# Performance work log

Hardware: AMD Instinct MI355X
Metric: run time of the kernel (lower is better)

## Reference

```python
import jax, jax.numpy as jnp
import numpy as np

EPS_BIAS = 1e-6  # bias_epsilon

def _l2n(x, axis):
    # F.normalize: x / clamp_min(||x||, 1e-12)
    return x / jnp.maximum(jnp.linalg.norm(x, axis=axis, keepdims=True), 1e-12)

def _se3_W(w):
    # convex completion: rows sum to 1
    return jnp.concatenate([w, 1.0 - w.sum(-1, keepdims=True)], axis=-1)

def _vlin(v, W):
    # channel-mixing linear over dim 1 of [B, C, 3, N]
    return jnp.einsum('oc,bcdn->bodn', W, v)

def _vec_sub(v, w, b, se3):
    # sub VecLinear with s_in=s_out=0: linear + tiny normalized bias
    W = _se3_W(w) if se3 else w
    out = _vlin(v, W)
    bias = (_l2n(b, -1) * EPS_BIAS).reshape(1, -1, 1, 1)
    return out + bias

def _cev_norm(x):
    # channel_equi_vec_normalize
    d = _l2n(x, 2)
    n = jnp.linalg.norm(x, axis=2, keepdims=True)
    return d * _l2n(n, 1)

def setup_inputs() -> dict:
    key = jax.random.key(0)
    B, v_in, v_out, s_in, s_out, N = 8, 128, 128, 64, 64, 4096
    ks = jax.random.split(key, 16)
    def w(k, shape, fan):
        return jax.random.normal(k, shape, jnp.float32) / np.float32(np.sqrt(fan))
    return {
        'v_input': jax.random.normal(ks[0], (B, v_in, 3, N), jnp.float32),
        's_input': jax.random.normal(ks[1], (B, s_in, N), jnp.float32),
        'weight':   w(ks[2], (v_out, v_in - 1), v_in) + 1.0 / v_in,
        'sv_w':     w(ks[3], (v_out, s_in), s_in),
        'sv_b':     w(ks[4], (v_out,), s_in),
        'cross_w':  w(ks[5], (v_out, v_in - 1), v_in) + 1.0 / v_in,
        'cross_b':  jax.random.normal(ks[6], (v_out,), jnp.float32),
        'crossfc_w': w(ks[7], (v_out, 2 * v_out - 1), 2 * v_out) + 1.0 / (2 * v_out),
        'crossfc_b': jax.random.normal(ks[8], (v_out,), jnp.float32),
        'vsdir_w':  w(ks[9], (v_in, v_in), v_in),
        'vsdir_b':  jax.random.normal(ks[10], (v_in,), jnp.float32),
        'vs_w':     w(ks[11], (s_out, v_in), v_in),
        'vs_b':     w(ks[12], (s_out,), v_in),
        'ss_w':     w(ks[13], (s_out, s_in), s_in),
        'ss_b':     w(ks[14], (s_out,), s_in),
    }

def reference(v_input, s_input, weight, sv_w, sv_b, cross_w, cross_b,
              crossfc_w, crossfc_b, vsdir_w, vsdir_b, vs_w, vs_b, ss_w, ss_b):
    # --- vector linear (sim3/se3: convex weights) ---
    v_o = _vlin(v_input, _se3_W(weight))                      # [B, v_out, 3, N]
    # --- scalar -> vector invariant scale (normalized over channels) ---
    scale = jnp.einsum('os,bsn->bon', sv_w, s_input) + sv_b[None, :, None]
    scale = _l2n(scale, 1)                                    # [B, v_out, N]
    m = v_o.mean(axis=1, keepdims=True)
    v_o = (v_o - m) * scale[:, :, None, :] + m
    # --- cross-product branch ---
    v_dual = _vec_sub(v_input, cross_w, cross_b, True)
    dual_o = v_dual.mean(axis=1, keepdims=True)
    out_o = v_o.mean(axis=1, keepdims=True)
    v_cross = jnp.cross(_cev_norm(v_dual - dual_o), v_o - out_o, axis=2) + v_o
    v_o = _vec_sub(jnp.concatenate([v_cross, v_o], axis=1), crossfc_w, crossfc_b, True)
    # --- vector -> scalar (invariant) ---
    v_sR = v_input - v_input.mean(axis=1, keepdims=True)
    dual_dir = _l2n(_vec_sub(v_sR, vsdir_w, vsdir_b, False), 2)  # so3 sub-module
    s_from_v = _l2n((v_sR * dual_dir).sum(axis=2), 1)         # [B, v_in, N]
    s_from_v = jnp.einsum('oc,bcn->bon', vs_w, s_from_v) + vs_b[None, :, None]
    s_from_s = jnp.einsum('os,bsn->bon', ss_w, s_input) + ss_b[None, :, None]
    return v_o, s_from_s + s_from_v
```

## Files before the change

### kernel.cpp

```cpp
#include <hip/hip_runtime.h>

#define VOUT_ELEMS 12582912

typedef __attribute__((ext_vector_type(8))) short bf16x8;
typedef __attribute__((ext_vector_type(4))) float f32x4;

__device__ __forceinline__ unsigned short f2b(float f) {
  unsigned x = __float_as_uint(f);
  x = (x + 0x7FFFu + ((x >> 16) & 1u)) >> 16;
  return (unsigned short)x;
}
__device__ __forceinline__ float b2f(unsigned short u) {
  return __uint_as_float(((unsigned)u) << 16);
}
__device__ __forceinline__ unsigned pk2(float a, float b) {
  unsigned r;
  asm("v_cvt_pk_bf16_f32 %0, %1, %2" : "=v"(r) : "v"(a), "v"(b));
  return r;
}


__global__ void kprep0(const float* __restrict__ weight, const float* __restrict__ cross_w,
                       const float* __restrict__ crossfc_w, const float* __restrict__ vsdir_w,
                       const float* __restrict__ cross_b, const float* __restrict__ crossfc_b,
                       const float* __restrict__ vsdir_b, float* __restrict__ wsf)
{
  const int tid = threadIdx.x;
  const int l = tid & 63;
  const int wg = blockIdx.x*4 + (tid>>6);
#pragma unroll
  for (int k = 0; k < 2; ++k) {
    int o = wg*2 + k;
    float a = weight[o*127+l]  + ((l<63) ? weight[o*127+64+l]  : 0.f);
    float b = cross_w[o*127+l] + ((l<63) ? cross_w[o*127+64+l] : 0.f);
    float f = crossfc_w[o*255+l] + crossfc_w[o*255+64+l] + crossfc_w[o*255+128+l]
            + ((l<63) ? crossfc_w[o*255+192+l] : 0.f);
    float v = vsdir_w[o*128+l] + vsdir_w[o*128+64+l];
#pragma unroll
    for (int m = 1; m < 64; m <<= 1) {
      a += __shfl_xor(a,m,64); b += __shfl_xor(b,m,64);
      f += __shfl_xor(f,m,64); v += __shfl_xor(v,m,64);
    }
    if (l == 0) {
      wsf[384+o] = a; wsf[512+o] = b; wsf[640+o] = f; wsf[768+o] = v*(1.f/128.f);
    }
  }
  if (blockIdx.x == 0 && tid < 192) {
    const float* bsrc = (tid < 64) ? cross_b : (tid < 128 ? crossfc_b : vsdir_b);
    float a = 0.f;
    for (int i = l; i < 128; i += 64) { float t = bsrc[i]; a += t*t; }
#pragma unroll
    for (int m = 1; m < 64; m <<= 1) a += __shfl_xor(a,m,64);
    float nb = fmaxf(sqrtf(a), 1e-12f);
    for (int i = l; i < 128; i += 64)
      wsf[(tid>>6)*128 + i] = bsrc[i] / nb * 1e-6f;
  }
}

__global__ void kprep1(const float* __restrict__ weight, const float* __restrict__ sv_w,
                       const float* __restrict__ cross_w, const float* __restrict__ crossfc_w,
                       const float* __restrict__ vsdir_w, const float* __restrict__ vs_w,
                       const float* __restrict__ ss_w,
                       unsigned short* __restrict__ wsb, const float* __restrict__ wsf)
{
  const int stride = 64*256;
  const int base = blockIdx.x*256 + threadIdx.x;
  const float* rs1 = wsf+384; const float* rs2 = wsf+512;
  const float* rsF = wsf+640; const float* vdm = wsf+768;
  for (int i = base; i < 16384; i += stride) {
    int j=i&7, lane=(i>>3)&63, ks=(i>>9)&3, mt=i>>11;
    int o=16*mt+(lane&15), cc=32*ks+8*(lane>>4)+j;
    wsb[i]       = f2b(cc<127 ? weight[o*127+cc]  : 1.f-rs1[o]);
    wsb[16384+i] = f2b(cc<127 ? cross_w[o*127+cc] : 1.f-rs2[o]);
    wsb[65536+i] = f2b(vsdir_w[o*128+cc] - vdm[o]);
  }
  for (int i = base; i < 32768; i += stride) {
    int j=i&7, lane=(i>>3)&63, ks=(i>>9)&7, mt=i>>12;
    int o=16*mt+(lane&15), cc=32*ks+8*(lane>>4)+j;
    wsb[32768+i] = f2b(cc<255 ? crossfc_w[o*255+cc] : 1.f-rsF[o]);
  }
  for (int i = base; i < 8192; i += stride) {
    int j=i&7, lane=(i>>3)&63, ks=(i>>9)&1, mt=i>>10;
    int o=16*mt+(lane&15), s=32*ks+8*(lane>>4)+j;
    wsb[81920+i] = f2b(sv_w[o*64+s]);
  }
  for (int i = base; i < 8192; i += stride) {
    int j=i&7, lane=(i>>3)&63, ks=(i>>9)&3, mt=i>>11;
    int o=16*mt+(lane&15), c=32*ks+8*(lane>>4)+j;
    wsb[90112+i] = f2b(vs_w[o*128+c]);
  }
  for (int i = base; i < 4096; i += stride) {
    int j=i&7, lane=(i>>3)&63, ks=(i>>9)&1, mt=i>>10;
    int o=16*mt+(lane&15), s=32*ks+8*(lane>>4)+j;
    wsb[98304+i] = f2b(ss_w[o*64+s]);
  }
}

__global__ __launch_bounds__(512) __attribute__((amdgpu_waves_per_eu(4)))
void kmain(
    const float* __restrict__ v_in, const float* __restrict__ s_in,
    const float* __restrict__ sv_b, const float* __restrict__ vs_b,
    const float* __restrict__ ss_b,
    const unsigned short* __restrict__ wsb, const float* __restrict__ wsf,
    float* __restrict__ out_v, float* __restrict__ out_s)
{
  __shared__ __align__(16) unsigned char smem[32768];
  unsigned short* bfr = (unsigned short*)smem;
  float* gmx          = (float*)(smem + 12288);
  float (*gred)[16][8]  = (float(*)[16][8])(smem + 12480);
  unsigned short* sfr = (unsigned short*)(smem + 24576);
  unsigned short* vfr = (unsigned short*)(smem + 26624);
  float (*gred2)[16][8] = (float(*)[16][8])(smem + 30720);

  const int tid = threadIdx.x;
  const int w = tid >> 6, l = tid & 63, h = l >> 4, c15 = l & 15;
  const int n0 = blockIdx.x * 16;
  const size_t bb = blockIdx.y;
  const size_t vbase = bb*384*4096 + n0;
  const size_t sbase = bb*64*4096 + n0;

  if (tid < 384) {
    int i = tid;
    int q = i & 3, d = (i >> 2) % 3, cq = i / 12;
    const float* src = &v_in[vbase + (size_t)(4*cq*3 + d)*4096 + 4*q];
    float4 x0 = *(const float4*)(src);
    float4 x1 = *(const float4*)(src + 3*4096);
    float4 x2 = *(const float4*)(src + 6*4096);
    float4 x3 = *(const float4*)(src + 9*4096);
    int slot = (cq >> 3)*3 + d;
    int hh = (cq >> 1) & 3;
    int jp = 2*(cq & 1);
    unsigned* bp = (unsigned*)bfr + (slot*64 + 16*hh + 4*q)*4 + jp;
    float a0[4]={x0.x,x0.y,x0.z,x0.w}, a1[4]={x1.x,x1.y,x1.z,x1.w};
    float a2[4]={x2.x,x2.y,x2.z,x2.w}, a3[4]={x3.x,x3.y,x3.z,x3.w};
#pragma unroll
    for (int e=0;e<4;++e)
      *(uint2*)(bp + e*4) = make_uint2(pk2(a0[e],a1[e]), pk2(a2[e],a3[e]));
  } else if (tid < 448) {
    int st = tid - 384;
    int q = st & 3, sq = st >> 2;
    const float* src = &s_in[sbase + (size_t)(4*sq)*4096 + 4*q];
    float4 x0 = *(const float4*)(src);
    float4 x1 = *(const float4*)(src + 4096);
    float4 x2 = *(const float4*)(src + 2*4096);
    float4 x3 = *(const float4*)(src + 3*4096);
    int slot = sq >> 3;
    int hh = (sq >> 1) & 3;
    int jp = 2*(sq & 1);
    unsigned* bp = (unsigned*)sfr + (slot*64 + 16*hh + 4*q)*4 + jp;
    float a0[4]={x0.x,x0.y,x0.z,x0.w}, a1[4]={x1.x,x1.y,x1.z,x1.w};
    float a2[4]={x2.x,x2.y,x2.z,x2.w}, a3[4]={x3.x,x3.y,x3.z,x3.w};
#pragma unroll
    for (int e=0;e<4;++e)
      *(uint2*)(bp + e*4) = make_uint2(pk2(a0[e],a1[e]), pk2(a2[e],a3[e]));
  }
  __syncthreads();

  const bf16x8* bv  = (const bf16x8*)bfr;
  const bf16x8* sfv_p = (const bf16x8*)sfr;
  const bf16x8* vfv_p = (const bf16x8*)vfr;
  const bf16x8* wv  = (const bf16x8*)wsb;
  const int obA = 16*w + 4*h;

  f32x4 avo[3], adu[3], adr[3], asc;
  {
    f32x4 b2A = *(const f32x4*)&wsf[obA];
    f32x4 bdA = *(const f32x4*)&wsf[256+obA];
#pragma unroll
    for (int d=0;d<3;++d) {
      avo[d]=(f32x4){0.f,0.f,0.f,0.f};
      adu[d]=b2A;
      adr[d]=bdA;
    }
    asc = *(const f32x4*)&sv_b[obA];
  }
#pragma unroll
  for (int ks=0;ks<4;++ks) {
    bf16x8 bx[3];
#pragma unroll
    for (int d=0;d<3;++d) bx[d] = bv[(ks*3+d)*64 + l];
    int fa = w*4 + ks;
    bf16x8 a1 = wv[fa*64 + l];
    bf16x8 a2 = wv[2048 + fa*64 + l];
    bf16x8 a3 = wv[8192 + fa*64 + l];
#pragma unroll
    for (int d=0;d<3;++d) {
      avo[d] = __builtin_amdgcn_mfma_f32_16x16x32_bf16(a1, bx[d], avo[d], 0,0,0);
      adu[d] = __builtin_amdgcn_mfma_f32_16x16x32_bf16(a2, bx[d], adu[d], 0,0,0);
      adr[d] = __builtin_amdgcn_mfma_f32_16x16x32_bf16(a3, bx[d], adr[d], 0,0,0);
    }
  }
#pragma unroll
  for (int ks=0;ks<2;++ks) {
    bf16x8 a4 = wv[10240 + (w*2+ks)*64 + l];
    asc = __builtin_amdgcn_mfma_f32_16x16x32_bf16(a4, sfv_p[ks*64+l], asc, 0,0,0);
  }
  if (w < 3) {
    bf16x8 aone;
#pragma unroll
    for (int j=0;j<8;++j) aone[j] = (short)0x3C00;
    f32x4 amx = (f32x4){0.f,0.f,0.f,0.f};
#pragma unroll
    for (int ks=0;ks<4;++ks)
      amx = __builtin_amdgcn_mfma_f32_16x16x32_bf16(aone, bv[(ks*3+w)*64+l], amx, 0,0,0);
    if (h==0) gmx[16*w + c15] = amx[0];
  }

  {
    float red[8];
#pragma unroll
    for (int d=0;d<3;++d) {
      red[d]   = avo[d][0]+avo[d][1]+avo[d][2]+avo[d][3];
      red[3+d] = adu[d][0]+adu[d][1]+adu[d][2]+adu[d][3];
    }
    float q2 = 0.f;
#pragma unroll
    for (int d=0;d<3;++d)
#pragma unroll
      for (int r=0;r<4;++r) q2 += adu[d][r]*adu[d][r];
    red[6] = q2;
    red[7] = asc[0]*asc[0]+asc[1]*asc[1]+asc[2]*asc[2]+asc[3]*asc[3];
#pragma unroll
    for (int m=16;m<64;m<<=1)
#pragma unroll
      for (int i=0;i<8;++i) red[i] += __shfl_xor(red[i], m, 64);
    if (h==0)
#pragma unroll
      for (int i=0;i<8;++i) gred[i][c15][w] = red[i];
  }
  __syncthreads();

  float mvo[3], mdu[3], mxv[3], d2s, sinv;
#pragma unroll
  for (int d=0;d<3;++d) {
    const f32x4* p  = (const f32x4*)gred[d][c15];
    const f32x4* p2 = (const f32x4*)gred[3+d][c15];
    f32x4 t0=p[0], t1=p[1], u0=p2[0], u1=p2[1];
    mvo[d] = (t0[0]+t0[1]+t0[2]+t0[3]+t1[0]+t1[1]+t1[2]+t1[3]) * (1.f/128.f);
    mdu[d] = (u0[0]+u0[1]+u0[2]+u0[3]+u1[0]+u1[1]+u1[2]+u1[3]) * (1.f/128.f);
    mxv[d] = gmx[16*d + c15];
  }
  { const f32x4* p = (const f32x4*)gred[6][c15];
    f32x4 t0=p[0], t1=p[1];
    d2s = t0[0]+t0[1]+t0[2]+t0[3]+t1[0]+t1[1]+t1[2]+t1[3]; }
  { const f32x4* p = (const f32x4*)gred[7][c15];
    f32x4 t0=p[0], t1=p[1];
    sinv = 1.f / fmaxf(sqrtf(t0[0]+t0[1]+t0[2]+t0[3]+t1[0]+t1[1]+t1[2]+t1[3]), 1e-12f); }

  float po[3] = {0.f,0.f,0.f};
#pragma unroll
  for (int r=0;r<4;++r) {
    float sk = asc[r] * sinv;
#pragma unroll
    for (int d=0;d<3;++d) {
      float t = (avo[d][r]-mvo[d])*sk + mvo[d];
      avo[d][r] = t;
      po[d] += t;
    }
  }

  const int ksq = w >> 1;
  const int hh2 = 2*(w&1) + (h>>1);
  const int ju = 2*(h&1);
  float sfvv[4]; float pfn = 0.f;
  {
    float xr[3][4];
#pragma unroll
    for (int d=0;d<3;++d) {
      uint2 u = *(const uint2*)((const unsigned*)bfr + ((ksq*3+d)*64 + 16*hh2 + c15)*4 + ju);
      xr[d][0]=b2f((unsigned short)u.x);  xr[d][1]=b2f((unsigned short)(u.x>>16));
      xr[d][2]=b2f((unsigned short)u.y);  xr[d][3]=b2f((unsigned short)(u.y>>16));
    }
#pragma unroll
    for (int r=0;r<4;++r) {
      float dx=adr[0][r], dy=adr[1][r], dz=adr[2][r];
      float rn = sqrtf(dx*dx+dy*dy+dz*dz);
      float inv = 1.f/fmaxf(rn,1e-12f);
      float vx = xr[0][r]-mxv[0], vy = xr[1][r]-mxv[1], vz = xr[2][r]-mxv[2];
      float dot = (vx*dx+vy*dy+vz*dz)*inv;
      sfvv[r] = dot; pfn += dot*dot;
    }
  }

  {
    float red2[4] = {po[0], po[1], po[2], pfn};
#pragma unroll
    for (int m=16;m<64;m<<=1)
#pragma unroll
      for (int i=0;i<4;++i) red2[i] += __shfl_xor(red2[i], m, 64);
    if (h==0)
#pragma unroll
      for (int i=0;i<4;++i) gred2[i][c15][w] = red2[i];
  }
  __syncthreads();

  float moo[3], sfni;
#pragma unroll
  for (int d=0;d<3;++d) {
    const f32x4* p = (const f32x4*)gred2[d][c15];
    f32x4 t0=p[0], t1=p[1];
    moo[d] = (t0[0]+t0[1]+t0[2]+t0[3]+t1[0]+t1[1]+t1[2]+t1[3]) * (1.f/128.f);
  }
  { const f32x4* p = (const f32x4*)gred2[3][c15];
    f32x4 t0=p[0], t1=p[1];
    sfni = 1.f/fmaxf(sqrtf(t0[0]+t0[1]+t0[2]+t0[3]+t1[0]+t1[1]+t1[2]+t1[3]), 1e-12f); }

  float m2 = mdu[0]*mdu[0]+mdu[1]*mdu[1]+mdu[2]*mdu[2];
  float F  = sqrtf(fmaxf(d2s - 128.f*m2, 0.f));
  float Fi = 1.f/fmaxf(F, 1e-12f);
  {
    *(uint2*)((unsigned*)vfr + (ksq*64 + 16*hh2 + c15)*4 + ju) =
      make_uint2(pk2(sfvv[0]*sfni, sfvv[1]*sfni),
                 pk2(sfvv[2]*sfni, sfvv[3]*sfni));
    float cv[3][4];
#pragma unroll
    for (int r=0;r<4;++r) {
      float ax=adu[0][r]-mdu[0], ay=adu[1][r]-mdu[1], az=adu[2][r]-mdu[2];
      float rn = sqrtf(ax*ax+ay*ay+az*az);
      float s1 = (rn*Fi)/fmaxf(rn,1e-12f);
      ax*=s1; ay*=s1; az*=s1;
      float bx=avo[0][r]-moo[0], by=avo[1][r]-moo[1], bz=avo[2][r]-moo[2];
      cv[0][r]=ay*bz-az*by+avo[0][r];
      cv[1][r]=az*bx-ax*bz+avo[1][r];
      cv[2][r]=ax*by-ay*bx+avo[2][r];
    }
#pragma unroll
    for (int d=0;d<3;++d) {
      *(uint2*)((unsigned*)bfr + ((ksq*3+d)*64 + 16*hh2 + c15)*4 + ju) =
        make_uint2(pk2(cv[d][0],cv[d][1]), pk2(cv[d][2],cv[d][3]));
      *(uint2*)((unsigned*)bfr + (((4+ksq)*3+d)*64 + 16*hh2 + c15)*4 + ju) =
        make_uint2(pk2(avo[d][0],avo[d][1]), pk2(avo[d][2],avo[d][3]));
    }
  }
  __syncthreads();

  f32x4 afc[3];
  {
    f32x4 bfA = *(const f32x4*)&wsf[128+obA];
#pragma unroll
    for (int d=0;d<3;++d) afc[d]=bfA;
  }
#pragma unroll
  for (int ks=0;ks<8;++ks) {
    bf16x8 bx[3];
#pragma unroll
    for (int d=0;d<3;++d) bx[d] = bv[(ks*3+d)*64 + l];
    bf16x8 a5 = wv[4096 + (w*8+ks)*64 + l];
#pragma unroll
    for (int d=0;d<3;++d)
      afc[d] = __builtin_amdgcn_mfma_f32_16x16x32_bf16(a5, bx[d], afc[d], 0,0,0);
  }
  if (w < 4) {
    f32x4 as2;
    {
      f32x4 bv1 = *(const f32x4*)&vs_b[obA];
      f32x4 bv2 = *(const f32x4*)&ss_b[obA];
      as2 = (f32x4){bv1[0]+bv2[0], bv1[1]+bv2[1], bv1[2]+bv2[2], bv1[3]+bv2[3]};
    }
#pragma unroll
    for (int ks=0;ks<4;++ks) {
      bf16x8 a6 = wv[11264 + (w*4+ks)*64 + l];
      as2 = __builtin_amdgcn_mfma_f32_16x16x32_bf16(a6, vfv_p[ks*64+l], as2, 0,0,0);
    }
#pragma unroll
    for (int ks=0;ks<2;++ks) {
      bf16x8 a7 = wv[12288 + (w*2+ks)*64 + l];
      as2 = __builtin_amdgcn_mfma_f32_16x16x32_bf16(a7, sfv_p[ks*64+l], as2, 0,0,0);
    }
#pragma unroll
    for (int r=0;r<4;++r)
      out_s[sbase + (size_t)(obA+r)*4096 + c15] = as2[r];
  }

#pragma unroll
  for (int d=0;d<3;++d)
#pragma unroll
    for (int r=0;r<4;++r)
      out_v[vbase + (size_t)((obA+r)*3 + d)*4096 + c15] = afc[d][r];
}

extern "C" void kernel_launch(void* const* d_in, const int* in_sizes, int n_in,
                              void* d_out, int out_size, void* d_ws, size_t ws_size,
                              hipStream_t stream) {
  (void)in_sizes; (void)n_in; (void)out_size; (void)ws_size;
  const float* v_in      = (const float*)d_in[0];
  const float* s_in      = (const float*)d_in[1];
  const float* weight    = (const float*)d_in[2];
  const float* sv_w      = (const float*)d_in[3];
  const float* sv_b      = (const float*)d_in[4];
  const float* cross_w   = (const float*)d_in[5];
  const float* cross_b   = (const float*)d_in[6];
  const float* crossfc_w = (const float*)d_in[7];
  const float* crossfc_b = (const float*)d_in[8];
  const float* vsdir_w   = (const float*)d_in[9];
  const float* vsdir_b   = (const float*)d_in[10];
  const float* vs_w      = (const float*)d_in[11];
  const float* vs_b      = (const float*)d_in[12];
  const float* ss_w      = (const float*)d_in[13];
  const float* ss_b      = (const float*)d_in[14];

  unsigned short* wsb = (unsigned short*)d_ws;
  float* wsf = (float*)((char*)d_ws + 204800);

  kprep0<<<16, 256, 0, stream>>>(weight, cross_w, crossfc_w, vsdir_w,
                                 cross_b, crossfc_b, vsdir_b, wsf);
  kprep1<<<64, 256, 0, stream>>>(weight, sv_w, cross_w, crossfc_w, vsdir_w,
                                 vs_w, ss_w, wsb, wsf);
  dim3 grid(4096/16, 8);
  kmain<<<grid, 512, 0, stream>>>(v_in, s_in, sv_b, vs_b, ss_b, wsb, wsf,
                                  (float*)d_out, (float*)d_out + VOUT_ELEMS);
}
```

Before: 64.21 us.

## Remove second block barrier by algebraic mean of scaled vectors and deferred norm

```diff
diff --git a/kernel.cpp b/kernel.cpp
--- a/kernel.cpp
+++ b/kernel.cpp
@@ -104,13 +104,12 @@
     const unsigned short* __restrict__ wsb, const float* __restrict__ wsf,
     float* __restrict__ out_v, float* __restrict__ out_s)
 {
-  __shared__ __align__(16) unsigned char smem[32768];
+  __shared__ __align__(16) unsigned char smem[38912];
   unsigned short* bfr = (unsigned short*)smem;
-  float* gmx          = (float*)(smem + 12288);
-  float (*gred)[16][8]  = (float(*)[16][8])(smem + 12480);
   unsigned short* sfr = (unsigned short*)(smem + 24576);
   unsigned short* vfr = (unsigned short*)(smem + 26624);
-  float (*gred2)[16][8] = (float(*)[16][8])(smem + 30720);
+  float (*gred)[16][8]  = (float(*)[16][8])(smem + 30720);
+  float (*gred2)[8]     = (float(*)[8])(smem + 38400);
 
   const int tid = threadIdx.x;
   const int w = tid >> 6, l = tid & 63, h = l >> 4, c15 = l & 15;
@@ -161,6 +160,9 @@
   const bf16x8* vfv_p = (const bf16x8*)vfr;
   const bf16x8* wv  = (const bf16x8*)wsb;
   const int obA = 16*w + 4*h;
+  const int ksq = w >> 1;
+  const int hh2 = 2*(w&1) + (h>>1);
+  const int ju = 2*(h&1);
 
   f32x4 avo[3], adu[3], adr[3], asc;
   {
@@ -195,23 +197,23 @@
     bf16x8 a4 = wv[10240 + (w*2+ks)*64 + l];
     asc = __builtin_amdgcn_mfma_f32_16x16x32_bf16(a4, sfv_p[ks*64+l], asc, 0,0,0);
   }
-  if (w < 3) {
-    bf16x8 aone;
-#pragma unroll
-    for (int j=0;j<8;++j) aone[j] = (short)0x3C00;
-    f32x4 amx = (f32x4){0.f,0.f,0.f,0.f};
-#pragma unroll
-    for (int ks=0;ks<4;++ks)
-      amx = __builtin_amdgcn_mfma_f32_16x16x32_bf16(aone, bv[(ks*3+w)*64+l], amx, 0,0,0);
-    if (h==0) gmx[16*w + c15] = amx[0];
+
+  float xr[3][4];
+#pragma unroll
+  for (int d=0;d<3;++d) {
+    uint2 u = *(const uint2*)((const unsigned*)bfr + ((ksq*3+d)*64 + 16*hh2 + c15)*4 + ju);
+    xr[d][0]=b2f((unsigned short)u.x);  xr[d][1]=b2f((unsigned short)(u.x>>16));
+    xr[d][2]=b2f((unsigned short)u.y);  xr[d][3]=b2f((unsigned short)(u.y>>16));
   }
 
   {
-    float red[8];
+    float red[15];
 #pragma unroll
     for (int d=0;d<3;++d) {
       red[d]   = avo[d][0]+avo[d][1]+avo[d][2]+avo[d][3];
       red[3+d] = adu[d][0]+adu[d][1]+adu[d][2]+adu[d][3];
+      red[8+d] = avo[d][0]*asc[0]+avo[d][1]*asc[1]+avo[d][2]*asc[2]+avo[d][3]*asc[3];
+      red[12+d]= xr[d][0]+xr[d][1]+xr[d][2]+xr[d][3];
     }
     float q2 = 0.f;
 #pragma unroll
@@ -220,98 +222,71 @@
       for (int r=0;r<4;++r) q2 += adu[d][r]*adu[d][r];
     red[6] = q2;
     red[7] = asc[0]*asc[0]+asc[1]*asc[1]+asc[2]*asc[2]+asc[3]*asc[3];
+    red[11]= asc[0]+asc[1]+asc[2]+asc[3];
 #pragma unroll
     for (int m=16;m<64;m<<=1)
 #pragma unroll
-      for (int i=0;i<8;++i) red[i] += __shfl_xor(red[i], m, 64);
+      for (int i=0;i<15;++i) red[i] += __shfl_xor(red[i], m, 64);
     if (h==0)
 #pragma unroll
-      for (int i=0;i<8;++i) gred[i][c15][w] = red[i];
+      for (int i=0;i<15;++i) gred[i][c15][w] = red[i];
   }
   __syncthreads();
 
-  float mvo[3], mdu[3], mxv[3], d2s, sinv;
+  float mvo[3], mdu[3], mxv[3], moo[3], d2s, sinv, Sa;
+  { const f32x4* p = (const f32x4*)gred[7][c15];
+    f32x4 t0=p[0], t1=p[1];
+    sinv = 1.f / fmaxf(sqrtf(t0[0]+t0[1]+t0[2]+t0[3]+t1[0]+t1[1]+t1[2]+t1[3]), 1e-12f); }
+  { const f32x4* p = (const f32x4*)gred[11][c15];
+    f32x4 t0=p[0], t1=p[1];
+    Sa = t0[0]+t0[1]+t0[2]+t0[3]+t1[0]+t1[1]+t1[2]+t1[3]; }
+  { const f32x4* p = (const f32x4*)gred[6][c15];
+    f32x4 t0=p[0], t1=p[1];
+    d2s = t0[0]+t0[1]+t0[2]+t0[3]+t1[0]+t1[1]+t1[2]+t1[3]; }
 #pragma unroll
   for (int d=0;d<3;++d) {
     const f32x4* p  = (const f32x4*)gred[d][c15];
     const f32x4* p2 = (const f32x4*)gred[3+d][c15];
-    f32x4 t0=p[0], t1=p[1], u0=p2[0], u1=p2[1];
+    const f32x4* p3 = (const f32x4*)gred[8+d][c15];
+    const f32x4* p4 = (const f32x4*)gred[12+d][c15];
+    f32x4 t0=p[0],  t1=p[1];
+    f32x4 u0=p2[0], u1=p2[1];
+    f32x4 v0=p3[0], v1=p3[1];
+    f32x4 x0=p4[0], x1=p4[1];
     mvo[d] = (t0[0]+t0[1]+t0[2]+t0[3]+t1[0]+t1[1]+t1[2]+t1[3]) * (1.f/128.f);
     mdu[d] = (u0[0]+u0[1]+u0[2]+u0[3]+u1[0]+u1[1]+u1[2]+u1[3]) * (1.f/128.f);
-    mxv[d] = gmx[16*d + c15];
-  }
-  { const f32x4* p = (const f32x4*)gred[6][c15];
-    f32x4 t0=p[0], t1=p[1];
-    d2s = t0[0]+t0[1]+t0[2]+t0[3]+t1[0]+t1[1]+t1[2]+t1[3]; }
-  { const f32x4* p = (const f32x4*)gred[7][c15];
-    f32x4 t0=p[0], t1=p[1];
-    sinv = 1.f / fmaxf(sqrtf(t0[0]+t0[1]+t0[2]+t0[3]+t1[0]+t1[1]+t1[2]+t1[3]), 1e-12f); }
-
-  float po[3] = {0.f,0.f,0.f};
+    float Svs = v0[0]+v0[1]+v0[2]+v0[3]+v1[0]+v1[1]+v1[2]+v1[3];
+    moo[d] = mvo[d] + sinv*(Svs - mvo[d]*Sa)*(1.f/128.f);
+    mxv[d] = (x0[0]+x0[1]+x0[2]+x0[3]+x1[0]+x1[1]+x1[2]+x1[3]) * (1.f/128.f);
+  }
+
 #pragma unroll
   for (int r=0;r<4;++r) {
     float sk = asc[r] * sinv;
 #pragma unroll
-    for (int d=0;d<3;++d) {
-      float t = (avo[d][r]-mvo[d])*sk + mvo[d];
-      avo[d][r] = t;
-      po[d] += t;
-    }
-  }
-
-  const int ksq = w >> 1;
-  const int hh2 = 2*(w&1) + (h>>1);
-  const int ju = 2*(h&1);
+    for (int d=0;d<3;++d)
+      avo[d][r] = (avo[d][r]-mvo[d])*sk + mvo[d];
+  }
+
   float sfvv[4]; float pfn = 0.f;
-  {
-    float xr[3][4];
-#pragma unroll
-    for (int d=0;d<3;++d) {
-      uint2 u = *(const uint2*)((const unsigned*)bfr + ((ksq*3+d)*64 + 16*hh2 + c15)*4 + ju);
-      xr[d][0]=b2f((unsigned short)u.x);  xr[d][1]=b2f((unsigned short)(u.x>>16));
-      xr[d][2]=b2f((unsigned short)u.y);  xr[d][3]=b2f((unsigned short)(u.y>>16));
-    }
-#pragma unroll
-    for (int r=0;r<4;++r) {
-      float dx=adr[0][r], dy=adr[1][r], dz=adr[2][r];
-      float rn = sqrtf(dx*dx+dy*dy+dz*dz);
-      float inv = 1.f/fmaxf(rn,1e-12f);
-      float vx = xr[0][r]-mxv[0], vy = xr[1][r]-mxv[1], vz = xr[2][r]-mxv[2];
-      float dot = (vx*dx+vy*dy+vz*dz)*inv;
-      sfvv[r] = dot; pfn += dot*dot;
-    }
-  }
-
-  {
-    float red2[4] = {po[0], po[1], po[2], pfn};
-#pragma unroll
-    for (int m=16;m<64;m<<=1)
-#pragma unroll
-      for (int i=0;i<4;++i) red2[i] += __shfl_xor(red2[i], m, 64);
-    if (h==0)
-#pragma unroll
-      for (int i=0;i<4;++i) gred2[i][c15][w] = red2[i];
-  }
-  __syncthreads();
-
-  float moo[3], sfni;
-#pragma unroll
-  for (int d=0;d<3;++d) {
-    const f32x4* p = (const f32x4*)gred2[d][c15];
-    f32x4 t0=p[0], t1=p[1];
-    moo[d] = (t0[0]+t0[1]+t0[2]+t0[3]+t1[0]+t1[1]+t1[2]+t1[3]) * (1.f/128.f);
-  }
-  { const f32x4* p = (const f32x4*)gred2[3][c15];
-    f32x4 t0=p[0], t1=p[1];
-    sfni = 1.f/fmaxf(sqrtf(t0[0]+t0[1]+t0[2]+t0[3]+t1[0]+t1[1]+t1[2]+t1[3]), 1e-12f); }
+#pragma unroll
+  for (int r=0;r<4;++r) {
+    float dx=adr[0][r], dy=adr[1][r], dz=adr[2][r];
+    float rn = sqrtf(dx*dx+dy*dy+dz*dz);
+    float inv = 1.f/fmaxf(rn,1e-12f);
+    float vx = xr[0][r]-mxv[0], vy = xr[1][r]-mxv[1], vz = xr[2][r]-mxv[2];
+    float dot = (vx*dx+vy*dy+vz*dz)*inv;
+    sfvv[r] = dot; pfn += dot*dot;
+  }
+  pfn += __shfl_xor(pfn,16,64); pfn += __shfl_xor(pfn,32,64);
+  if (h==0) gred2[c15][w] = pfn;
 
   float m2 = mdu[0]*mdu[0]+mdu[1]*mdu[1]+mdu[2]*mdu[2];
   float F  = sqrtf(fmaxf(d2s - 128.f*m2, 0.f));
   float Fi = 1.f/fmaxf(F, 1e-12f);
   {
     *(uint2*)((unsigned*)vfr + (ksq*64 + 16*hh2 + c15)*4 + ju) =
-      make_uint2(pk2(sfvv[0]*sfni, sfvv[1]*sfni),
-                 pk2(sfvv[2]*sfni, sfvv[3]*sfni));
+      make_uint2(pk2(sfvv[0], sfvv[1]), pk2(sfvv[2], sfvv[3]));
     float cv[3][4];
 #pragma unroll
     for (int r=0;r<4;++r) {
@@ -357,19 +332,24 @@
       f32x4 bv2 = *(const f32x4*)&ss_b[obA];
       as2 = (f32x4){bv1[0]+bv2[0], bv1[1]+bv2[1], bv1[2]+bv2[2], bv1[3]+bv2[3]};
     }
+    f32x4 asv = (f32x4){0.f,0.f,0.f,0.f};
 #pragma unroll
     for (int ks=0;ks<4;++ks) {
       bf16x8 a6 = wv[11264 + (w*4+ks)*64 + l];
-      as2 = __builtin_amdgcn_mfma_f32_16x16x32_bf16(a6, vfv_p[ks*64+l], as2, 0,0,0);
+      asv = __builtin_amdgcn_mfma_f32_16x16x32_bf16(a6, vfv_p[ks*64+l], asv, 0,0,0);
     }
 #pragma unroll
     for (int ks=0;ks<2;++ks) {
       bf16x8 a7 = wv[12288 + (w*2+ks)*64 + l];
       as2 = __builtin_amdgcn_mfma_f32_16x16x32_bf16(a7, sfv_p[ks*64+l], as2, 0,0,0);
     }
+    float sfni;
+    { const f32x4* p = (const f32x4*)gred2[c15];
+      f32x4 t0=p[0], t1=p[1];
+      sfni = 1.f/fmaxf(sqrtf(t0[0]+t0[1]+t0[2]+t0[3]+t1[0]+t1[1]+t1[2]+t1[3]), 1e-12f); }
 #pragma unroll
     for (int r=0;r<4;++r)
-      out_s[sbase + (size_t)(obA+r)*4096 + c15] = as2[r];
+      out_s[sbase + (size_t)(obA+r)*4096 + c15] = as2[r] + asv[r]*sfni;
   }
 
 #pragma unroll
```

New measurement: 94.33 us. 1.47x slower.
